# Optimization experiments

Measured on AMD Instinct MI355X. Metric: run time of the kernel, lower is better.

Reference implementation:

```python
import jax, jax.numpy as jnp
import numpy as np

B, S, D, H = 8, 512, 768, 12
DH = D // H  # head size 64


def setup_inputs() -> dict:
    key = jax.random.key(0)
    ks = jax.random.split(key, 24)
    std = D ** -0.5
    w = lambda k, shape: jax.random.normal(k, shape, jnp.float32) * std
    b = lambda k, n: jax.random.normal(k, (n,), jnp.float32) * 0.01
    return {
        "hidden_states": jax.random.normal(ks[0], (B, S, D), jnp.float32),
        "mol": jax.random.normal(ks[1], (B, S, D), jnp.float32),
        "Wq": w(ks[2], (D, D)), "bq": b(ks[3], D),
        "Wk": w(ks[4], (D, D)), "bk": b(ks[5], D),
        "Wv": w(ks[6], (D, D)), "bv": b(ks[7], D),
        "Wqm": w(ks[8], (D, D)), "bqm": b(ks[9], D),
        "Wkm": w(ks[10], (D, D)), "bkm": b(ks[11], D),
        "Wvm": w(ks[12], (D, D)), "bvm": b(ks[13], D),
        "Wfc": w(ks[14], (2 * D, D)), "bfc": b(ks[15], D),
        "Wfcm": w(ks[16], (2 * D, D)), "bfcm": b(ks[17], D),
        "Wo": w(ks[18], (D, D)), "bo": b(ks[19], D),
        "Wom": w(ks[20], (D, D)), "bom": b(ks[21], D),
    }


def _split_heads(x):
    # [B,S,D] -> [B,H,S,DH]
    b_, s_, _ = x.shape
    return x.reshape(b_, s_, H, DH).transpose(0, 2, 1, 3)


def _merge_heads(x):
    # [B,H,S,DH] -> [B,S,D]
    b_, _, s_, _ = x.shape
    return x.transpose(0, 2, 1, 3).reshape(b_, s_, H * DH)


def _attend(q, k, v):
    # q:[B,H,Sq,DH], k,v:[B,H,Sk,DH]  (dropout rate = 0 -> identity)
    scores = jnp.einsum('bhqd,bhkd->bhqk', q, k) / np.sqrt(DH).astype(np.float32)
    probs = jax.nn.softmax(scores, axis=-1)
    return _merge_heads(jnp.einsum('bhqk,bhkd->bhqd', probs, v))


def reference(hidden_states, mol, Wq, bq, Wk, bk, Wv, bv, Wqm, bqm, Wkm, bkm,
              Wvm, bvm, Wfc, bfc, Wfcm, bfcm, Wo, bo, Wom, bom):
    q = _split_heads(hidden_states @ Wq + bq)
    k = _split_heads(hidden_states @ Wk + bk)
    v = _split_heads(hidden_states @ Wv + bv)
    qm = _split_heads(mol @ Wqm + bqm)
    km = _split_heads(mol @ Wkm + bkm)
    vm = _split_heads(mol @ Wvm + bvm)

    # prot branch: self-attn (q over prot K/V) + guided attn (mol Q over prot K/V)
    a_pp = _attend(q, k, v)      # [B,S,D]
    a_mp = _attend(qm, k, v)     # [B,S,D]
    attn_prot = (jnp.concatenate([a_pp, a_mp], axis=-1) @ Wfc + bfc) @ Wo + bo

    # mol branch: self-attn (mol Q over mol K/V) + guided attn (prot Q over mol K/V)
    a_mm = _attend(qm, km, vm)
    a_pm = _attend(q, km, vm)
    attn_mol = (jnp.concatenate([a_mm, a_pm], axis=-1) @ Wfcm + bfcm) @ Wom + bom

    return attn_prot, attn_mol
```

## Files before the change

### kernel.cpp

```cpp
#include <hip/hip_runtime.h>
#include <math.h>

#define B_   8
#define S_   512
#define D_   768
#define H_   12
#define DH_  64
#define NTOK (B_*S_)
#define D2_  (2*D_)
#define ND_  ((size_t)NTOK * D_)
#define WSZ_ ((size_t)D_ * D_)
#define FSZ_ ((size_t)D2_ * D_)

typedef unsigned short ushortT;
typedef short bf16x8 __attribute__((ext_vector_type(8)));
typedef float f32x4  __attribute__((ext_vector_type(4)));
typedef unsigned int u32;

#define QSCL 0.1803368801111204f

__device__ __forceinline__ unsigned short f2bf(float f) {
    unsigned int x = __float_as_uint(f);
    unsigned int lsb = (x >> 16) & 1u;
    x += 0x7fffu + lsb;
    return (unsigned short)(x >> 16);
}
__device__ __forceinline__ u32 pkbf(float a, float b) {
    u32 ua = (__float_as_uint(a) + 0x8000u) >> 16;
    u32 ub = (__float_as_uint(b) + 0x8000u) & 0xffff0000u;
    return ua | ub;
}

#if __has_builtin(__builtin_amdgcn_exp2f)
#define EXP2(x) __builtin_amdgcn_exp2f(x)
#else
#define EXP2(x) exp2f(x)
#endif

__device__ __forceinline__ void ld_g2l16(const ushortT* g, ushortT* l) {
    __builtin_amdgcn_global_load_lds(
        (const __attribute__((address_space(1))) u32*)g,
        (__attribute__((address_space(3))) u32*)l, 16, 0, 0);
}

#define PREP_NBLK 13062
struct PrepJob {
    const float *hs, *mol, *Wfc, *Wfcm;
    ushortT *hsb, *molb, *Wfcb, *Wfcmb;
    const float* tw_in[8]; ushortT* tw_out[8]; float tw_scl[8];
    const float *bfc, *Wo, *bo, *bfcm, *Wom, *bom;
    float *bcoP, *bcoM;
};
__global__ __launch_bounds__(256) void prep_k(PrepJob pj)
{
    __shared__ float t[32][33];
    const int bx = blockIdx.x;
    const int tid = threadIdx.x;

    if (bx < 8448) {
        const float* in; ushortT* out; int base;
        if (bx < 3072)      { in = pj.hs;   out = pj.hsb;   base = 0; }
        else if (bx < 6144) { in = pj.mol;  out = pj.molb;  base = 3072; }
        else if (bx < 7296) { in = pj.Wfc;  out = pj.Wfcb;  base = 6144; }
        else                { in = pj.Wfcm; out = pj.Wfcmb; base = 7296; }
        size_t i = ((size_t)(bx - base) * 256 + tid) * 4;
        float4 f = *(const float4*)(in + i);
        ushort4 u;
        u.x = f2bf(f.x); u.y = f2bf(f.y); u.z = f2bf(f.z); u.w = f2bf(f.w);
        *(ushort4*)(out + i) = u;
    } else if (bx < 13056) {
        int sub = bx - 8448;
        int z = sub / 576, r = sub - z * 576;
        int by = r / 24, bxx = r - by * 24;
        const float* __restrict__ in = pj.tw_in[z];
        ushortT* __restrict__ out = pj.tw_out[z];
        const float scl = pj.tw_scl[z];
        const int r0 = by * 32, c0 = bxx * 32;
        const int x = tid & 31, y = tid >> 5;
        #pragma unroll
        for (int i = 0; i < 4; ++i)
            t[y + 8 * i][x] = in[(size_t)(r0 + y + 8 * i) * D_ + c0 + x];
        __syncthreads();
        #pragma unroll
        for (int i = 0; i < 4; ++i)
            out[(size_t)(c0 + y + 8 * i) * D_ + r0 + x] = f2bf(t[x][y + 8 * i] * scl);
    } else {
        int b = bx - 13056;
        int zb = b / 3;
        int n = (b - zb * 3) * 256 + tid;
        const float* bf_ = zb ? pj.bfcm : pj.bfc;
        const float* W_  = zb ? pj.Wom : pj.Wo;
        const float* bo_ = zb ? pj.bom : pj.bo;
        float* o_ = zb ? pj.bcoM : pj.bcoP;
        float s = bo_[n];
        #pragma unroll 8
        for (int j = 0; j < D_; ++j) s += bf_[j] * W_[(size_t)j * D_ + n];
        o_[n] = s;
    }
}

struct GJob {
    const ushortT* X;
    const ushortT* Wt;
    const float*   bias;
    float          bscale;
    void*          Y;
    int            nx;
    int            nblk;
    int            ldy;
    int            flags;
};
struct GJobs { GJob j[8]; };
__global__ __launch_bounds__(256) void gemm_flat(GJobs gjs, int K)
{
    __shared__ __attribute__((aligned(16))) ushortT At[128 * 64];
    __shared__ __attribute__((aligned(16))) ushortT Bt[128 * 64];

    int bx = blockIdx.x;
    int ji = 0;
    while (bx >= gjs.j[ji].nblk) { bx -= gjs.j[ji].nblk; ++ji; }
    const ushortT* __restrict__ X  = gjs.j[ji].X;
    const ushortT* __restrict__ Wt = gjs.j[ji].Wt;
    const float* __restrict__ bias = gjs.j[ji].bias;
    const float bscale = gjs.j[ji].bscale;
    void* Y        = gjs.j[ji].Y;
    const int nx   = gjs.j[ji].nx;
    const int ldy  = gjs.j[ji].ldy;
    const int flags= gjs.j[ji].flags;

    const int by = bx / nx, bxx = bx - by * nx;
    const int bm = by * 128, bn = bxx * 128;

    const int tid = threadIdx.x;
    const int lane = tid & 63, wave = tid >> 6;
    const int quad = lane >> 4, l16 = lane & 15;
    const int wm = wave >> 1, wn = wave & 1;

    f32x4 acc[4][4];
    #pragma unroll
    for (int i = 0; i < 4; ++i)
        #pragma unroll
        for (int j = 0; j < 4; ++j)
            acc[i][j] = (f32x4){0.f, 0.f, 0.f, 0.f};

    const int crow = tid >> 3;
    const int cko  = ((tid & 7) ^ (crow & 7)) * 8;
    int px[2];
    px[0] = ((quad) ^ (l16 & 7)) * 8;
    px[1] = ((4 + quad) ^ (l16 & 7)) * 8;

    const ushortT* gX = X + (size_t)(bm + crow) * K + cko;
    const ushortT* gW = Wt + (size_t)(bn + crow) * K + cko;

    for (int k0 = 0; k0 < K; k0 += 64) {
        __syncthreads();
        #pragma unroll
        for (int i = 0; i < 4; ++i) {
            const int s = tid + i * 256;
            ld_g2l16(gX + (size_t)(i * 32) * K + k0, &At[s * 8]);
            ld_g2l16(gW + (size_t)(i * 32) * K + k0, &Bt[s * 8]);
        }
        __syncthreads();

        #pragma unroll
        for (int kc = 0; kc < 2; ++kc) {
            bf16x8 af[4], bf[4];
            #pragma unroll
            for (int mt = 0; mt < 4; ++mt)
                af[mt] = *(const bf16x8*)&At[(wm * 64 + mt * 16 + l16) * 64 + px[kc]];
            #pragma unroll
            for (int nt = 0; nt < 4; ++nt)
                bf[nt] = *(const bf16x8*)&Bt[(wn * 64 + nt * 16 + l16) * 64 + px[kc]];
            #pragma unroll
            for (int mt = 0; mt < 4; ++mt)
                #pragma unroll
                for (int nt = 0; nt < 4; ++nt)
                    acc[mt][nt] = __builtin_amdgcn_mfma_f32_16x16x32_bf16(af[mt], bf[nt], acc[mt][nt], 0, 0, 0);
        }
    }

    const int row0 = bm + wm * 64, col0 = bn + wn * 64;
    #pragma unroll
    for (int mt = 0; mt < 4; ++mt) {
        #pragma unroll
        for (int nt = 0; nt < 4; ++nt) {
            const int col = col0 + nt * 16 + l16;
            const float bval = (flags & 2) ? bias[col] * bscale : 0.f;
            #pragma unroll
            for (int r = 0; r < 4; ++r) {
                const int row = row0 + mt * 16 + quad * 4 + r;
                float vsum = acc[mt][nt][r] + bval;
                if (flags & 1) ((float*)Y)[(size_t)row * ldy + col] = vsum;
                else           ((ushortT*)Y)[(size_t)row * ldy + col] = f2bf(vsum);
            }
        }
    }
}

__global__ __launch_bounds__(256) void transpose_v(
    const ushortT* __restrict__ v, const ushortT* __restrict__ vm,
    ushortT* __restrict__ vt, ushortT* __restrict__ vmt)
{
    __shared__ ushortT t[64][65];
    const ushortT* __restrict__ in = blockIdx.z ? vm : v;
    ushortT* __restrict__ out = blockIdx.z ? vmt : vt;
    const int bh = blockIdx.y, b = bh / H_, h = bh % H_;
    const int s0 = blockIdx.x * 64;
    const int c4 = threadIdx.x & 15, r = threadIdx.x >> 4;
    #pragma unroll
    for (int i = 0; i < 4; ++i) {
        int row = r + 16 * i;
        ushort4 u = *(const ushort4*)(in + (size_t)(b * S_ + s0 + row) * D_ + h * DH_ + c4 * 4);
        t[row][c4 * 4 + 0] = u.x; t[row][c4 * 4 + 1] = u.y;
        t[row][c4 * 4 + 2] = u.z; t[row][c4 * 4 + 3] = u.w;
    }
    __syncthreads();
    #pragma unroll
    for (int i = 0; i < 4; ++i) {
        int d = r + 16 * i;
        ushort4 u;
        u.x = t[c4 * 4 + 0][d]; u.y = t[c4 * 4 + 1][d];
        u.z = t[c4 * 4 + 2][d]; u.w = t[c4 * 4 + 3][d];
        *(ushort4*)(out + (size_t)(bh * DH_ + d) * S_ + s0 + c4 * 4) = u;
    }
}

__global__ __launch_bounds__(256) void attn_mfma(
    const ushortT* __restrict__ q,  const ushortT* __restrict__ k,
    const ushortT* __restrict__ vt, const ushortT* __restrict__ qm,
    const ushortT* __restrict__ km, const ushortT* __restrict__ vmt,
    ushortT* __restrict__ catP, ushortT* __restrict__ catM)
{
    __shared__ __attribute__((aligned(16))) ushortT Kt0[64 * 32], Kt1[64 * 32];
    __shared__ __attribute__((aligned(16))) ushortT Vt0[64 * 32], Vt1[64 * 32];
    __shared__ __attribute__((aligned(16))) ushortT Pt0[4][32 * 32], Pt1[4][32 * 32];

    const int tid = threadIdx.x;
    const int lane = tid & 63, wave = tid >> 6;
    const int quad = lane >> 4, l16 = lane & 15;
    const int bh = blockIdx.y, b = bh / H_, h = bh % H_;
    const int q0w = blockIdx.x * 128 + wave * 32;

    const ushortT *Q, *Kp, *Vp;
    ushortT* Out;
    int colbase;
    switch (blockIdx.z) {
        case 0:  Q = q;  Kp = k;  Vp = vt;  Out = catP; colbase = 0;  break;
        case 1:  Q = qm; Kp = k;  Vp = vt;  Out = catP; colbase = D_; break;
        case 2:  Q = qm; Kp = km; Vp = vmt; Out = catM; colbase = 0;  break;
        default: Q = q;  Kp = km; Vp = vmt; Out = catM; colbase = D_; break;
    }

    bf16x8 Qf[2][2];
    #pragma unroll
    for (int mt = 0; mt < 2; ++mt)
        #pragma unroll
        for (int kc = 0; kc < 2; ++kc)
            Qf[mt][kc] = *(const bf16x8*)(Q + (size_t)(b * S_ + q0w + mt * 16 + l16) * D_
                                            + h * DH_ + kc * 32 + quad * 8);

    f32x4 OT[4][2];
    #pragma unroll
    for (int dt = 0; dt < 4; ++dt)
        #pragma unroll
        for (int mt = 0; mt < 2; ++mt)
            OT[dt][mt] = (f32x4){0.f, 0.f, 0.f, 0.f};
    float lrun[2] = {0.f, 0.f};

    const int drow = tid >> 2;
    const int dcl  = ((tid & 3) ^ ((drow >> 1) & 3)) * 8;
    const ushortT* gK = Kp + (size_t)(b * S_) * D_ + h * DH_ + (size_t)drow * D_ + dcl;
    const ushortT* gV = Vp + (size_t)bh * DH_ * S_ + (size_t)drow * S_ + dcl;

    const int swl = (l16 >> 1) & 3;
    const int rdo = (quad ^ swl) * 8;
    int roff[4];
    #pragma unroll
    for (int t = 0; t < 4; ++t) roff[t] = (t * 16 + l16) * 32 + rdo;
    int wpoff[2][2];
    #pragma unroll
    for (int mt = 0; mt < 2; ++mt)
        #pragma unroll
        for (int kb = 0; kb < 2; ++kb)
            wpoff[mt][kb] = (mt * 16 + l16) * 32 + (((kb * 2 + (quad >> 1)) ^ swl) * 8) + (quad & 1) * 4;

    for (int kt = 0; kt < S_; kt += 64) {
        __syncthreads();
        ld_g2l16(gK,      &Kt0[tid * 8]);
        ld_g2l16(gK + 32, &Kt1[tid * 8]);
        ld_g2l16(gV,      &Vt0[tid * 8]);
        ld_g2l16(gV + 32, &Vt1[tid * 8]);
        gK += (size_t)64 * D_;
        gV += 64;
        __syncthreads();

        f32x4 St[4][2];
        #pragma unroll
        for (int ktl = 0; ktl < 4; ++ktl)
            #pragma unroll
            for (int mt = 0; mt < 2; ++mt)
                St[ktl][mt] = (f32x4){0.f, 0.f, 0.f, 0.f};
        #pragma unroll
        for (int ktl = 0; ktl < 4; ++ktl) {
            bf16x8 ka0 = *(const bf16x8*)&Kt0[roff[ktl]];
            bf16x8 ka1 = *(const bf16x8*)&Kt1[roff[ktl]];
            #pragma unroll
            for (int mt = 0; mt < 2; ++mt) {
                St[ktl][mt] = __builtin_amdgcn_mfma_f32_16x16x32_bf16(ka0, Qf[mt][0], St[ktl][mt], 0, 0, 0);
                St[ktl][mt] = __builtin_amdgcn_mfma_f32_16x16x32_bf16(ka1, Qf[mt][1], St[ktl][mt], 0, 0, 0);
            }
        }

        #pragma unroll
        for (int mt = 0; mt < 2; ++mt) {
            float rs = 0.f;
            #pragma unroll
            for (int ktl = 0; ktl < 4; ++ktl) {
                float p0 = EXP2(St[ktl][mt][0]);
                float p1 = EXP2(St[ktl][mt][1]);
                float p2 = EXP2(St[ktl][mt][2]);
                float p3 = EXP2(St[ktl][mt][3]);
                rs += (p0 + p1) + (p2 + p3);
                uint2 u = make_uint2(pkbf(p0, p1), pkbf(p2, p3));
                if (ktl < 2) *(uint2*)&Pt0[wave][wpoff[mt][ktl & 1]] = u;
                else         *(uint2*)&Pt1[wave][wpoff[mt][ktl & 1]] = u;
            }
            lrun[mt] += rs;
        }

        bf16x8 Pb[2][2];
        #pragma unroll
        for (int mt = 0; mt < 2; ++mt) {
            Pb[mt][0] = *(const bf16x8*)&Pt0[wave][(mt * 16 + l16) * 32 + rdo];
            Pb[mt][1] = *(const bf16x8*)&Pt1[wave][(mt * 16 + l16) * 32 + rdo];
        }
        #pragma unroll
        for (int dt = 0; dt < 4; ++dt) {
            bf16x8 va0 = *(const bf16x8*)&Vt0[roff[dt]];
            bf16x8 va1 = *(const bf16x8*)&Vt1[roff[dt]];
            #pragma unroll
            for (int mt = 0; mt < 2; ++mt) {
                OT[dt][mt] = __builtin_amdgcn_mfma_f32_16x16x32_bf16(va0, Pb[mt][0], OT[dt][mt], 0, 0, 0);
                OT[dt][mt] = __builtin_amdgcn_mfma_f32_16x16x32_bf16(va1, Pb[mt][1], OT[dt][mt], 0, 0, 0);
            }
        }
    }

    #pragma unroll
    for (int mt = 0; mt < 2; ++mt) {
        float l = lrun[mt];
        l += __shfl_xor(l, 16, 64);
        l += __shfl_xor(l, 32, 64);
        const float inv = 1.f / l;
        ushortT* yp = Out + (size_t)(b * S_ + q0w + mt * 16 + l16) * D2_ + colbase + h * DH_;
        #pragma unroll
        for (int dt = 0; dt < 4; ++dt) {
            uint2 u = make_uint2(pkbf(OT[dt][mt][0] * inv, OT[dt][mt][1] * inv),
                                 pkbf(OT[dt][mt][2] * inv, OT[dt][mt][3] * inv));
            *(uint2*)(yp + dt * 16 + quad * 4) = u;
        }
    }
}

extern "C" void kernel_launch(void* const* d_in, const int* in_sizes, int n_in,
                              void* d_out, int out_size, void* d_ws, size_t ws_size,
                              hipStream_t stream) {
    const float* hs   = (const float*)d_in[0];
    const float* mol  = (const float*)d_in[1];
    const float* Wq   = (const float*)d_in[2];
    const float* bq   = (const float*)d_in[3];
    const float* Wk   = (const float*)d_in[4];
    const float* bk   = (const float*)d_in[5];
    const float* Wv   = (const float*)d_in[6];
    const float* bv   = (const float*)d_in[7];
    const float* Wqm  = (const float*)d_in[8];
    const float* bqm  = (const float*)d_in[9];
    const float* Wkm  = (const float*)d_in[10];
    const float* bkm  = (const float*)d_in[11];
    const float* Wvm  = (const float*)d_in[12];
    const float* bvm  = (const float*)d_in[13];
    const float* Wfc  = (const float*)d_in[14];
    const float* bfc  = (const float*)d_in[15];
    const float* Wfcm = (const float*)d_in[16];
    const float* bfcm = (const float*)d_in[17];
    const float* Wo   = (const float*)d_in[18];
    const float* bo   = (const float*)d_in[19];
    const float* Wom  = (const float*)d_in[20];
    const float* bom  = (const float*)d_in[21];

    float* out = (float*)d_out;
    ushortT* ws = (ushortT*)d_ws;

    ushortT* hsb   = ws;
    ushortT* molb  = hsb + ND_;
    ushortT* Wfcb  = molb + ND_;
    ushortT* Wfcmb = Wfcb + FSZ_;
    ushortT* WqT   = Wfcmb + FSZ_;
    ushortT* WkT   = WqT + WSZ_;
    ushortT* WvT   = WkT + WSZ_;
    ushortT* WqmT  = WvT + WSZ_;
    ushortT* WkmT  = WqmT + WSZ_;
    ushortT* WvmT  = WkmT + WSZ_;
    ushortT* WoT   = WvmT + WSZ_;
    ushortT* WomT  = WoT + WSZ_;
    ushortT* WcoT  = WomT + WSZ_;
    ushortT* WcomT = WcoT + FSZ_;
    ushortT* q     = WcomT + FSZ_;
    ushortT* k     = q + ND_;
    ushortT* v     = k + ND_;
    ushortT* qm    = v + ND_;
    ushortT* km    = qm + ND_;
    ushortT* vm    = km + ND_;
    ushortT* vtr   = vm + ND_;
    ushortT* vmtr  = vtr + ND_;
    ushortT* catP  = vmtr + ND_;
    ushortT* catM  = catP + 2 * ND_;
    float*   bcoP  = (float*)(catM + 2 * ND_);
    float*   bcoM  = bcoP + D_;

    {
        PrepJob pj;
        pj.hs = hs; pj.mol = mol; pj.Wfc = Wfc; pj.Wfcm = Wfcm;
        pj.hsb = hsb; pj.molb = molb; pj.Wfcb = Wfcb; pj.Wfcmb = Wfcmb;
        const float* wi[8] = {Wq, Wk, Wv, Wqm, Wkm, Wvm, Wo, Wom};
        ushortT* wo_[8]    = {WqT, WkT, WvT, WqmT, WkmT, WvmT, WoT, WomT};
        const float sc[8]  = {QSCL, 1.f, 1.f, QSCL, 1.f, 1.f, 1.f, 1.f};
        for (int i = 0; i < 8; ++i) { pj.tw_in[i] = wi[i]; pj.tw_out[i] = wo_[i]; pj.tw_scl[i] = sc[i]; }
        pj.bfc = bfc; pj.Wo = Wo; pj.bo = bo; pj.bfcm = bfcm; pj.Wom = Wom; pj.bom = bom;
        pj.bcoP = bcoP; pj.bcoM = bcoM;
        prep_k<<<dim3(PREP_NBLK), 256, 0, stream>>>(pj);
    }

    {
        GJobs gj = {};
        gj.j[0] = {WoT,  Wfcb,  nullptr, 1.f,  WcoT,  12, 72,  D2_, 0};
        gj.j[1] = {WomT, Wfcmb, nullptr, 1.f,  WcomT, 12, 72,  D2_, 0};
        gj.j[2] = {hsb,  WqT,  bq,  QSCL, q,  6, 192, D_, 2};
        gj.j[3] = {hsb,  WkT,  bk,  1.f,  k,  6, 192, D_, 2};
        gj.j[4] = {hsb,  WvT,  bv,  1.f,  v,  6, 192, D_, 2};
        gj.j[5] = {molb, WqmT, bqm, QSCL, qm, 6, 192, D_, 2};
        gj.j[6] = {molb, WkmT, bkm, 1.f,  km, 6, 192, D_, 2};
        gj.j[7] = {molb, WvmT, bvm, 1.f,  vm, 6, 192, D_, 2};
        gemm_flat<<<dim3(72 * 2 + 192 * 6), 256, 0, stream>>>(gj, D_);
    }

    transpose_v<<<dim3(S_ / 64, B_ * H_, 2), 256, 0, stream>>>(v, vm, vtr, vmtr);

    attn_mfma<<<dim3(S_ / 128, B_ * H_, 4), 256, 0, stream>>>(q, k, vtr, qm, km, vmtr, catP, catM);

    {
        GJobs gj = {};
        gj.j[0] = {catP, WcoT,  bcoP, 1.f, out,       6, 192, D_, 3};
        gj.j[1] = {catM, WcomT, bcoM, 1.f, out + ND_, 6, 192, D_, 3};
        gemm_flat<<<dim3(192 * 2), 256, 0, stream>>>(gj, D2_);
    }
}
```

Measured before the change: 302.8 us.

## Fuse QKV projections, write V transposed in epilogue, parallelize bias folding

The three Q/K/V projections per input become one GEMM with N=2304 over the contiguous transposed weights. Q and K are stored interleaved with row stride 2*D, and the V columns are written directly in head-transposed layout from the GEMM epilogue. This removes the separate transpose_v kernel and its extra read/write pass, at the cost of more scattered 8-byte stores. The serial bfc·Wo bias fold is moved out of the prep kernel into 32 extra GEMM blocks that each handle a chunk and combine results with atomicAdd. The Q scale is now folded into a precomputed bias vector instead of being applied per output.

After: 280.0 us. 7.5% less time.

```diff
diff --git a/kernel.cpp b/kernel.cpp
--- a/kernel.cpp
+++ b/kernel.cpp
@@ -8,6 +8,7 @@
 #define DH_  64
 #define NTOK (B_*S_)
 #define D2_  (2*D_)
+#define D3_  (3*D_)
 #define ND_  ((size_t)NTOK * D_)
 #define WSZ_ ((size_t)D_ * D_)
 #define FSZ_ ((size_t)D2_ * D_)
@@ -43,13 +44,14 @@
         (__attribute__((address_space(3))) u32*)l, 16, 0, 0);
 }
 
-#define PREP_NBLK 13062
+#define PREP_NBLK 13080
 struct PrepJob {
     const float *hs, *mol, *Wfc, *Wfcm;
     ushortT *hsb, *molb, *Wfcb, *Wfcmb;
     const float* tw_in[8]; ushortT* tw_out[8]; float tw_scl[8];
-    const float *bfc, *Wo, *bo, *bfcm, *Wom, *bom;
-    float *bcoP, *bcoM;
+    const float *bo, *bom;
+    const float *bq, *bk, *bv, *bqm, *bkm, *bvm;
+    float *bcoP, *bcoM, *bqkvP, *bqkvM;
 };
 __global__ __launch_bounds__(256) void prep_k(PrepJob pj)
 {
@@ -84,18 +86,23 @@
         #pragma unroll
         for (int i = 0; i < 4; ++i)
             out[(size_t)(c0 + y + 8 * i) * D_ + r0 + x] = f2bf(t[x][y + 8 * i] * scl);
+    } else if (bx < 13062) {
+        int i = bx - 13056;
+        int zb = i / 3;
+        int n = (i - zb * 3) * 256 + tid;
+        if (zb == 0) pj.bcoP[n] = pj.bo[n];
+        else         pj.bcoM[n] = pj.bom[n];
     } else {
-        int b = bx - 13056;
-        int zb = b / 3;
-        int n = (b - zb * 3) * 256 + tid;
-        const float* bf_ = zb ? pj.bfcm : pj.bfc;
-        const float* W_  = zb ? pj.Wom : pj.Wo;
-        const float* bo_ = zb ? pj.bom : pj.bo;
-        float* o_ = zb ? pj.bcoM : pj.bcoP;
-        float s = bo_[n];
-        #pragma unroll 8
-        for (int j = 0; j < D_; ++j) s += bf_[j] * W_[(size_t)j * D_ + n];
-        o_[n] = s;
+        int i = bx - 13062;
+        int z = i / 9;
+        int n = (i - z * 9) * 256 + tid;
+        int seg = n / D_, off = n - seg * D_;
+        float v;
+        if (z == 0)
+            v = (seg == 0) ? pj.bq[off] * QSCL : (seg == 1 ? pj.bk[off] : pj.bv[off]);
+        else
+            v = (seg == 0) ? pj.bqm[off] * QSCL : (seg == 1 ? pj.bkm[off] : pj.bvm[off]);
+        (z == 0 ? pj.bqkvP : pj.bqkvM)[n] = v;
     }
 }
 
@@ -103,27 +110,53 @@
     const ushortT* X;
     const ushortT* Wt;
     const float*   bias;
-    float          bscale;
     void*          Y;
+    ushortT*       Yv;
     int            nx;
     int            nblk;
     int            ldy;
     int            flags;
 };
-struct GJobs { GJob j[8]; };
-__global__ __launch_bounds__(256) void gemm_flat(GJobs gjs, int K)
+struct GJobs { GJob j[4]; };
+struct FoldArgs { const float *bfc, *Wo, *bfcm, *Wom; float *bcoP, *bcoM; };
+
+__global__ __launch_bounds__(256) void gemm_flat(GJobs gjs, FoldArgs fa, int K, int gemm_total)
 {
     __shared__ __attribute__((aligned(16))) ushortT At[128 * 64];
     __shared__ __attribute__((aligned(16))) ushortT Bt[128 * 64];
 
+    const int tid = threadIdx.x;
     int bx = blockIdx.x;
+
+    if (bx >= gemm_total) {
+        int fi = bx - gemm_total;
+        int zb = fi >> 4, chunk = fi & 15;
+        const float* bf_ = zb ? fa.bfcm : fa.bfc;
+        const float* W_  = zb ? fa.Wom : fa.Wo;
+        float* o_ = zb ? fa.bcoM : fa.bcoP;
+        float s0 = 0.f, s1 = 0.f, s2 = 0.f;
+        const int j0 = chunk * 48;
+        #pragma unroll 4
+        for (int j = j0; j < j0 + 48; ++j) {
+            float bv = bf_[j];
+            const float* row = W_ + (size_t)j * D_;
+            s0 += bv * row[tid];
+            s1 += bv * row[tid + 256];
+            s2 += bv * row[tid + 512];
+        }
+        atomicAdd(&o_[tid], s0);
+        atomicAdd(&o_[tid + 256], s1);
+        atomicAdd(&o_[tid + 512], s2);
+        return;
+    }
+
     int ji = 0;
     while (bx >= gjs.j[ji].nblk) { bx -= gjs.j[ji].nblk; ++ji; }
     const ushortT* __restrict__ X  = gjs.j[ji].X;
     const ushortT* __restrict__ Wt = gjs.j[ji].Wt;
     const float* __restrict__ bias = gjs.j[ji].bias;
-    const float bscale = gjs.j[ji].bscale;
     void* Y        = gjs.j[ji].Y;
+    ushortT* Yv    = gjs.j[ji].Yv;
     const int nx   = gjs.j[ji].nx;
     const int ldy  = gjs.j[ji].ldy;
     const int flags= gjs.j[ji].flags;
@@ -131,7 +164,6 @@
     const int by = bx / nx, bxx = bx - by * nx;
     const int bm = by * 128, bn = bxx * 128;
 
-    const int tid = threadIdx.x;
     const int lane = tid & 63, wave = tid >> 6;
     const int quad = lane >> 4, l16 = lane & 15;
     const int wm = wave >> 1, wn = wave & 1;
@@ -180,55 +212,45 @@
     }
 
     const int row0 = bm + wm * 64, col0 = bn + wn * 64;
-    #pragma unroll
-    for (int mt = 0; mt < 4; ++mt) {
-        #pragma unroll
-        for (int nt = 0; nt < 4; ++nt) {
-            const int col = col0 + nt * 16 + l16;
-            const float bval = (flags & 2) ? bias[col] * bscale : 0.f;
-            #pragma unroll
-            for (int r = 0; r < 4; ++r) {
-                const int row = row0 + mt * 16 + quad * 4 + r;
-                float vsum = acc[mt][nt][r] + bval;
-                if (flags & 1) ((float*)Y)[(size_t)row * ldy + col] = vsum;
-                else           ((ushortT*)Y)[(size_t)row * ldy + col] = f2bf(vsum);
+    if ((flags & 4) && bn >= D2_) {
+        const int bb = row0 >> 9, s0 = row0 & 511;
+        #pragma unroll
+        for (int mt = 0; mt < 4; ++mt) {
+            #pragma unroll
+            for (int nt = 0; nt < 4; ++nt) {
+                const int col = col0 + nt * 16 + l16;
+                const int cv = col - D2_;
+                const int hh = cv >> 6, dd = cv & 63;
+                const float bval = bias[col];
+                ushortT* vp = Yv + ((size_t)(bb * H_ + hh) * DH_ + dd) * S_
+                                 + s0 + mt * 16 + quad * 4;
+                uint2 u = make_uint2(pkbf(acc[mt][nt][0] + bval, acc[mt][nt][1] + bval),
+                                     pkbf(acc[mt][nt][2] + bval, acc[mt][nt][3] + bval));
+                *(uint2*)vp = u;
             }
         }
-    }
-}
-
-__global__ __launch_bounds__(256) void transpose_v(
-    const ushortT* __restrict__ v, const ushortT* __restrict__ vm,
-    ushortT* __restrict__ vt, ushortT* __restrict__ vmt)
-{
-    __shared__ ushortT t[64][65];
-    const ushortT* __restrict__ in = blockIdx.z ? vm : v;
-    ushortT* __restrict__ out = blockIdx.z ? vmt : vt;
-    const int bh = blockIdx.y, b = bh / H_, h = bh % H_;
-    const int s0 = blockIdx.x * 64;
-    const int c4 = threadIdx.x & 15, r = threadIdx.x >> 4;
-    #pragma unroll
-    for (int i = 0; i < 4; ++i) {
-        int row = r + 16 * i;
-        ushort4 u = *(const ushort4*)(in + (size_t)(b * S_ + s0 + row) * D_ + h * DH_ + c4 * 4);
-        t[row][c4 * 4 + 0] = u.x; t[row][c4 * 4 + 1] = u.y;
-        t[row][c4 * 4 + 2] = u.z; t[row][c4 * 4 + 3] = u.w;
-    }
-    __syncthreads();
-    #pragma unroll
-    for (int i = 0; i < 4; ++i) {
-        int d = r + 16 * i;
-        ushort4 u;
-        u.x = t[c4 * 4 + 0][d]; u.y = t[c4 * 4 + 1][d];
-        u.z = t[c4 * 4 + 2][d]; u.w = t[c4 * 4 + 3][d];
-        *(ushort4*)(out + (size_t)(bh * DH_ + d) * S_ + s0 + c4 * 4) = u;
+    } else {
+        #pragma unroll
+        for (int mt = 0; mt < 4; ++mt) {
+            #pragma unroll
+            for (int nt = 0; nt < 4; ++nt) {
+                const int col = col0 + nt * 16 + l16;
+                const float bval = (flags & 2) ? bias[col] : 0.f;
+                #pragma unroll
+                for (int r = 0; r < 4; ++r) {
+                    const int row = row0 + mt * 16 + quad * 4 + r;
+                    float vsum = acc[mt][nt][r] + bval;
+                    if (flags & 1) ((float*)Y)[(size_t)row * ldy + col] = vsum;
+                    else           ((ushortT*)Y)[(size_t)row * ldy + col] = f2bf(vsum);
+                }
+            }
+        }
     }
 }
 
 __global__ __launch_bounds__(256) void attn_mfma(
-    const ushortT* __restrict__ q,  const ushortT* __restrict__ k,
-    const ushortT* __restrict__ vt, const ushortT* __restrict__ qm,
-    const ushortT* __restrict__ km, const ushortT* __restrict__ vmt,
+    const ushortT* __restrict__ qkP, const ushortT* __restrict__ qkM,
+    const ushortT* __restrict__ vtP, const ushortT* __restrict__ vtM,
     ushortT* __restrict__ catP, ushortT* __restrict__ catM)
 {
     __shared__ __attribute__((aligned(16))) ushortT Kt0[64 * 32], Kt1[64 * 32];
@@ -245,10 +267,10 @@
     ushortT* Out;
     int colbase;
     switch (blockIdx.z) {
-        case 0:  Q = q;  Kp = k;  Vp = vt;  Out = catP; colbase = 0;  break;
-        case 1:  Q = qm; Kp = k;  Vp = vt;  Out = catP; colbase = D_; break;
-        case 2:  Q = qm; Kp = km; Vp = vmt; Out = catM; colbase = 0;  break;
-        default: Q = q;  Kp = km; Vp = vmt; Out = catM; colbase = D_; break;
+        case 0:  Q = qkP; Kp = qkP + D_; Vp = vtP; Out = catP; colbase = 0;  break;
+        case 1:  Q = qkM; Kp = qkP + D_; Vp = vtP; Out = catP; colbase = D_; break;
+        case 2:  Q = qkM; Kp = qkM + D_; Vp = vtM; Out = catM; colbase = 0;  break;
+        default: Q = qkP; Kp = qkM + D_; Vp = vtM; Out = catM; colbase = D_; break;
     }
 
     bf16x8 Qf[2][2];
@@ -256,7 +278,7 @@
     for (int mt = 0; mt < 2; ++mt)
         #pragma unroll
         for (int kc = 0; kc < 2; ++kc)
-            Qf[mt][kc] = *(const bf16x8*)(Q + (size_t)(b * S_ + q0w + mt * 16 + l16) * D_
+            Qf[mt][kc] = *(const bf16x8*)(Q + (size_t)(b * S_ + q0w + mt * 16 + l16) * D2_
                                             + h * DH_ + kc * 32 + quad * 8);
 
     f32x4 OT[4][2];
@@ -269,7 +291,7 @@
 
     const int drow = tid >> 2;
     const int dcl  = ((tid & 3) ^ ((drow >> 1) & 3)) * 8;
-    const ushortT* gK = Kp + (size_t)(b * S_) * D_ + h * DH_ + (size_t)drow * D_ + dcl;
+    const ushortT* gK = Kp + (size_t)(b * S_) * D2_ + h * DH_ + (size_t)drow * D2_ + dcl;
     const ushortT* gV = Vp + (size_t)bh * DH_ * S_ + (size_t)drow * S_ + dcl;
 
     const int swl = (l16 >> 1) & 3;
@@ -290,7 +312,7 @@
         ld_g2l16(gK + 32, &Kt1[tid * 8]);
         ld_g2l16(gV,      &Vt0[tid * 8]);
         ld_g2l16(gV + 32, &Vt1[tid * 8]);
-        gK += (size_t)64 * D_;
+        gK += (size_t)64 * D2_;
         gV += 64;
         __syncthreads();
 
@@ -405,18 +427,16 @@
     ushortT* WomT  = WoT + WSZ_;
     ushortT* WcoT  = WomT + WSZ_;
     ushortT* WcomT = WcoT + FSZ_;
-    ushortT* q     = WcomT + FSZ_;
-    ushortT* k     = q + ND_;
-    ushortT* v     = k + ND_;
-    ushortT* qm    = v + ND_;
-    ushortT* km    = qm + ND_;
-    ushortT* vm    = km + ND_;
-    ushortT* vtr   = vm + ND_;
-    ushortT* vmtr  = vtr + ND_;
-    ushortT* catP  = vmtr + ND_;
+    ushortT* qkP   = WcomT + FSZ_;
+    ushortT* qkM   = qkP + 2 * ND_;
+    ushortT* vtrP  = qkM + 2 * ND_;
+    ushortT* vtrM  = vtrP + ND_;
+    ushortT* catP  = vtrM + ND_;
     ushortT* catM  = catP + 2 * ND_;
     float*   bcoP  = (float*)(catM + 2 * ND_);
     float*   bcoM  = bcoP + D_;
+    float*   bqkvP = bcoM + D_;
+    float*   bqkvM = bqkvP + D3_;
 
     {
         PrepJob pj;
@@ -426,32 +446,31 @@
         ushortT* wo_[8]    = {WqT, WkT, WvT, WqmT, WkmT, WvmT, WoT, WomT};
         const float sc[8]  = {QSCL, 1.f, 1.f, QSCL, 1.f, 1.f, 1.f, 1.f};
         for (int i = 0; i < 8; ++i) { pj.tw_in[i] = wi[i]; pj.tw_out[i] = wo_[i]; pj.tw_scl[i] = sc[i]; }
-        pj.bfc = bfc; pj.Wo = Wo; pj.bo = bo; pj.bfcm = bfcm; pj.Wom = Wom; pj.bom = bom;
-        pj.bcoP = bcoP; pj.bcoM = bcoM;
+        pj.bo = bo; pj.bom = bom;
+        pj.bq = bq; pj.bk = bk; pj.bv = bv; pj.bqm = bqm; pj.bkm = bkm; pj.bvm = bvm;
+        pj.bcoP = bcoP; pj.bcoM = bcoM; pj.bqkvP = bqkvP; pj.bqkvM = bqkvM;
         prep_k<<<dim3(PREP_NBLK), 256, 0, stream>>>(pj);
     }
+
+    FoldArgs fa = {bfc, Wo, bfcm, Wom, bcoP, bcoM};
 
     {
         GJobs gj = {};
-        gj.j[0] = {WoT,  Wfcb,  nullptr, 1.f,  WcoT,  12, 72,  D2_, 0};
-        gj.j[1] = {WomT, Wfcmb, nullptr, 1.f,  WcomT, 12, 72,  D2_, 0};
-        gj.j[2] = {hsb,  WqT,  bq,  QSCL, q,  6, 192, D_, 2};
-        gj.j[3] = {hsb,  WkT,  bk,  1.f,  k,  6, 192, D_, 2};
-        gj.j[4] = {hsb,  WvT,  bv,  1.f,  v,  6, 192, D_, 2};
-        gj.j[5] = {molb, WqmT, bqm, QSCL, qm, 6, 192, D_, 2};
-        gj.j[6] = {molb, WkmT, bkm, 1.f,  km, 6, 192, D_, 2};
-        gj.j[7] = {molb, WvmT, bvm, 1.f,  vm, 6, 192, D_, 2};
-        gemm_flat<<<dim3(72 * 2 + 192 * 6), 256, 0, stream>>>(gj, D_);
-    }
-
-    transpose_v<<<dim3(S_ / 64, B_ * H_, 2), 256, 0, stream>>>(v, vm, vtr, vmtr);
-
-    attn_mfma<<<dim3(S_ / 128, B_ * H_, 4), 256, 0, stream>>>(q, k, vtr, qm, km, vmtr, catP, catM);
+        gj.j[0] = {hsb,  WqT,  bqkvP,  qkP,   vtrP, 18, 576, D2_, 2 | 4};
+        gj.j[1] = {molb, WqmT, bqkvM,  qkM,   vtrM, 18, 576, D2_, 2 | 4};
+        gj.j[2] = {WoT,  Wfcb,  nullptr, WcoT,  nullptr, 12, 72, D2_, 0};
+        gj.j[3] = {WomT, Wfcmb, nullptr, WcomT, nullptr, 12, 72, D2_, 0};
+        const int total = 576 + 576 + 72 + 72;
+        gemm_flat<<<dim3(total + 32), 256, 0, stream>>>(gj, fa, D_, total);
+    }
+
+    attn_mfma<<<dim3(S_ / 128, B_ * H_, 4), 256, 0, stream>>>(qkP, qkM, vtrP, vtrM, catP, catM);
 
     {
         GJobs gj = {};
-        gj.j[0] = {catP, WcoT,  bcoP, 1.f, out,       6, 192, D_, 3};
-        gj.j[1] = {catM, WcomT, bcoM, 1.f, out + ND_, 6, 192, D_, 3};
-        gemm_flat<<<dim3(192 * 2), 256, 0, stream>>>(gj, D2_);
-    }
-}
+        gj.j[0] = {catP, WcoT,  bcoP, out,       nullptr, 6, 192, D_, 3};
+        gj.j[1] = {catM, WcomT, bcoM, out + ND_, nullptr, 6, 192, D_, 3};
+        gj.j[2].nblk = 0x7fffffff; gj.j[3].nblk = 0x7fffffff;
+        gemm_flat<<<dim3(384), 256, 0, stream>>>(gj, fa, D2_, 384);
+    }
+}
```
